# Optimization experiments

Hardware: AMD Instinct MI355X
Metric: run time of the kernel (lower is better)

The kernel has to match this reference:

```python
import jax, jax.numpy as jnp
import numpy as np

N = 50000        # nodes
E = 600000       # edges (before self-loops)
VOCAB = 100000
EMB = 128
HID = 128
G = 64           # graphs in batch
NEG_SLOPE = 0.2


def setup_inputs() -> dict:
    key = jax.random.key(0)
    ks = jax.random.split(key, 16)
    x_idx = jax.random.randint(ks[0], (N,), 0, VOCAB)
    edge_index = jax.random.randint(ks[1], (2, E), 0, N)
    edge_attr = jax.random.uniform(ks[2], (E,), dtype=jnp.float32)
    batch = jnp.sort(jax.random.randint(ks[3], (N,), 0, G))
    # embedding table; padding_idx=0 row zeroed as in nn.Embedding(padding_idx=0)
    emb_table = (jax.random.normal(ks[4], (VOCAB, EMB), dtype=jnp.float32) * 0.05).at[0].set(0.0)
    glorot = lambda k, shp: jax.random.normal(k, shp, dtype=jnp.float32) * np.float32(np.sqrt(2.0 / sum(shp)))
    W1 = glorot(ks[5], (HID, EMB))
    att_src1 = glorot(ks[6], (HID,)) * 0.0 + jax.random.normal(ks[6], (HID,), dtype=jnp.float32) * np.float32(np.sqrt(2.0 / (HID + 1)))
    att_dst1 = jax.random.normal(ks[7], (HID,), dtype=jnp.float32) * np.float32(np.sqrt(2.0 / (HID + 1)))
    W2 = glorot(ks[8], (HID, HID))
    att_src2 = jax.random.normal(ks[9], (HID,), dtype=jnp.float32) * np.float32(np.sqrt(2.0 / (HID + 1)))
    att_dst2 = jax.random.normal(ks[10], (HID,), dtype=jnp.float32) * np.float32(np.sqrt(2.0 / (HID + 1)))
    W3 = glorot(ks[11], (HID // 2, HID))
    b3 = jnp.zeros((HID // 2,), jnp.float32)
    W4 = glorot(ks[12], (2, HID // 2))
    b4 = jnp.zeros((2,), jnp.float32)
    return {"x_idx": x_idx, "edge_index": edge_index, "edge_attr": edge_attr, "batch": batch,
            "emb_table": emb_table, "W1": W1, "att_src1": att_src1, "att_dst1": att_dst1,
            "W2": W2, "att_src2": att_src2, "att_dst2": att_dst2,
            "W3": W3, "b3": b3, "W4": W4, "b4": b4}


def _segment_softmax(logits, seg, n):
    m = jax.ops.segment_max(logits, seg, num_segments=n)
    e = jnp.exp(logits - m[seg])
    s = jax.ops.segment_sum(e, seg, num_segments=n)
    return e / (s[seg] + 1e-16)


def _edge_attr_gat_conv(x, src, dst, ea, W, a_src, a_dst, n):
    H = x @ W.T                                   # [n, out]
    # per-edge score: (H_i . a_dst) + (H_j . a_src); compute per-node then gather
    alpha = (H @ a_dst)[dst] + (H @ a_src)[src]   # [e]
    alpha = jnp.where(alpha >= 0, alpha, NEG_SLOPE * alpha)
    alpha = alpha * ea                            # multiplicative edge attr
    alpha = _segment_softmax(alpha, dst, n)       # softmax over in-neighborhoods
    return jax.ops.segment_sum(H[src] * alpha[:, None], dst, num_segments=n)


def reference(x_idx, edge_index, edge_attr, batch, emb_table,
              W1, att_src1, att_dst1, W2, att_src2, att_dst2, W3, b3, W4, b4):
    n = x_idx.shape[0]
    loops = jnp.arange(n)
    # add_self_loops (done inside each conv in torch; same edges both layers)
    src = jnp.concatenate([edge_index[0], loops])
    dst = jnp.concatenate([edge_index[1], loops])  # edge_index_i (aggregation index)
    ea = jnp.concatenate([edge_attr, jnp.ones((n,), edge_attr.dtype)])
    x = emb_table[x_idx]
    x = jax.nn.relu(_edge_attr_gat_conv(x, src, dst, ea, W1, att_src1, att_dst1, n))
    x = jax.nn.relu(_edge_attr_gat_conv(x, src, dst, ea, W2, att_src2, att_dst2, n))
    # global_mean_pool
    sums = jax.ops.segment_sum(x, batch, num_segments=G)
    counts = jax.ops.segment_sum(jnp.ones((n,), x.dtype), batch, num_segments=G)
    g = sums / jnp.maximum(counts, 1.0)[:, None]
    # MLP head (dropout = identity at eval)
    h = jax.nn.relu(g @ W3.T + b3)
    return h @ W4.T + b4
```

## Files before the change

### kernel.cpp

```cpp
#include <hip/hip_runtime.h>
#include <cstdint>
#include <cstddef>


#define CSR_CHUNK 8192
#define NXCD 8

__device__ __forceinline__ float wave_sum(float v) {
#pragma unroll
  for (int m = 32; m >= 1; m >>= 1) v += __shfl_xor(v, m, 64);
  return v;
}


__global__ void init_kernel(int* __restrict__ deg, float* __restrict__ gsum,
                            int* __restrict__ gstart, int* __restrict__ gend,
                            int N, int G) {
  int i = blockIdx.x * blockDim.x + threadIdx.x;
  if (i < N) deg[i] = 1;
  if (i < G * 128) gsum[i] = 0.f;
  if (i < G) { gstart[i] = 0; gend[i] = 0; }
}

__global__ void count_deg_part_kernel(const int* __restrict__ edge_index,
                                      int* __restrict__ deg, int E, int RN) {
  int r = blockIdx.x & (NXCD - 1);
  int s = blockIdx.x >> 3;
  int lo = r * RN, hi = lo + RN;
  int e1 = min(E, (s + 1) * CSR_CHUNK);
  for (int e = s * CSR_CHUNK + threadIdx.x; e < e1; e += blockDim.x) {
    int d = edge_index[E + e];
    if (d >= lo && d < hi) atomicAdd(&deg[d], 1);
  }
}

__global__ void scan1_kernel(const int* __restrict__ deg, int* __restrict__ bsum, int N) {
  __shared__ int ws[4];
  int tid = threadIdx.x;
  int i = blockIdx.x * 256 + tid;
  int v = (i < N) ? deg[i] : 0;
#pragma unroll
  for (int m = 32; m >= 1; m >>= 1) v += __shfl_xor(v, m, 64);
  if ((tid & 63) == 0) ws[tid >> 6] = v;
  __syncthreads();
  if (tid == 0) bsum[blockIdx.x] = ws[0] + ws[1] + ws[2] + ws[3];
}

__device__ __forceinline__ int block_excl_scan_256(int v, int tid, int* wsum) {
  int lane = tid & 63, wid = tid >> 6;
  int incl = v;
#pragma unroll
  for (int off = 1; off < 64; off <<= 1) {
    int t = __shfl_up(incl, off, 64);
    if (lane >= off) incl += t;
  }
  if (lane == 63) wsum[wid] = incl;
  __syncthreads();
  int woff = 0;
#pragma unroll
  for (int w = 0; w < 4; ++w)
    if (w < wid) woff += wsum[w];
  return woff + incl - v;
}

__global__ void scan2_kernel(const int* __restrict__ bsum, int* __restrict__ boff,
                             int* __restrict__ row_ptr, int nb, int N) {
  __shared__ int wsum[4];
  int tid = threadIdx.x;
  int v = (tid < nb) ? bsum[tid] : 0;
  int excl = block_excl_scan_256(v, tid, wsum);
  if (tid < nb) boff[tid] = excl;
  if (tid == 255) row_ptr[N] = excl + v;
}

__global__ void scan3_fill_kernel(const int* __restrict__ deg, const int* __restrict__ boff,
                                  int* __restrict__ row_ptr, int2* __restrict__ pk,
                                  int* __restrict__ cur, int N) {
  __shared__ int wsum[4];
  int tid = threadIdx.x;
  int i = blockIdx.x * 256 + tid;
  int v = (i < N) ? deg[i] : 0;
  int excl = block_excl_scan_256(v, tid, wsum);
  if (i < N) {
    int p = boff[blockIdx.x] + excl;
    row_ptr[i] = p;
    pk[p] = make_int2(i, __float_as_int(1.0f));
    cur[i] = p + 1;
  }
}

__global__ void fillB_part_kernel(const int* __restrict__ edge_index,
                                  const float* __restrict__ ea,
                                  int* __restrict__ cur, int2* __restrict__ pk,
                                  int E, int RN) {
  int r = blockIdx.x & (NXCD - 1);
  int s = blockIdx.x >> 3;
  int lo = r * RN, hi = lo + RN;
  int e1 = min(E, (s + 1) * CSR_CHUNK);
  for (int e = s * CSR_CHUNK + threadIdx.x; e < e1; e += blockDim.x) {
    int d = edge_index[E + e];
    if (d >= lo && d < hi) {
      int s0 = edge_index[e];
      float a0 = ea[e];
      int p = atomicAdd(&cur[d], 1);
      pk[p] = make_int2(s0, __float_as_int(a0));
    }
  }
}


__global__ __launch_bounds__(256) void gemm_att_kernel(
    const float* __restrict__ Xin, const int* __restrict__ gidx,
    const float* __restrict__ W,
    const float* __restrict__ a_src, const float* __restrict__ a_dst,
    float* __restrict__ H, float* __restrict__ sv, float* __restrict__ dv, int N) {
  __shared__ float XsT[32][64];
  __shared__ float Wt[32][128];
  __shared__ float av[2][128];

  int tid = threadIdx.x;
  int tx = tid & 15, ty = tid >> 4;
  int rb = blockIdx.x * 64;

  if (tid < 128) { av[0][tid] = a_src[tid]; av[1][tid] = a_dst[tid]; }

  int r0 = tid & 63;
  int q0 = tid >> 6;
  int gr0 = rb + r0; if (gr0 >= N) gr0 = N - 1;
  const float* rp0 = gidx ? (Xin + (size_t)gidx[gr0] * 128) : (Xin + (size_t)gr0 * 128);

  float acc[4][8];
#pragma unroll
  for (int r = 0; r < 4; ++r)
#pragma unroll
    for (int j = 0; j < 8; ++j) acc[r][j] = 0.f;

#pragma unroll
  for (int ks = 0; ks < 4; ++ks) {
    const int k0 = ks * 32;
    __syncthreads();
    {
      float4 v0 = *(const float4*)(rp0 + k0 + q0 * 4);
      float4 v1 = *(const float4*)(rp0 + k0 + (q0 + 4) * 4);
      XsT[q0 * 4 + 0][r0] = v0.x; XsT[q0 * 4 + 1][r0] = v0.y;
      XsT[q0 * 4 + 2][r0] = v0.z; XsT[q0 * 4 + 3][r0] = v0.w;
      XsT[(q0 + 4) * 4 + 0][r0] = v1.x; XsT[(q0 + 4) * 4 + 1][r0] = v1.y;
      XsT[(q0 + 4) * 4 + 2][r0] = v1.z; XsT[(q0 + 4) * 4 + 3][r0] = v1.w;
    }
#pragma unroll
    for (int it = 0; it < 4; ++it) {
      int idx = tid + it * 256;
      int c = idx & 127, q = idx >> 7;
      float4 v = *(const float4*)(W + (size_t)c * 128 + k0 + q * 4);
      Wt[q * 4 + 0][c] = v.x; Wt[q * 4 + 1][c] = v.y;
      Wt[q * 4 + 2][c] = v.z; Wt[q * 4 + 3][c] = v.w;
    }
    __syncthreads();
#pragma unroll 8
    for (int k = 0; k < 32; ++k) {
      float4 xa = *(const float4*)&XsT[k][ty * 4];
      float4 wl = *(const float4*)&Wt[k][tx * 4];
      float4 wh = *(const float4*)&Wt[k][tx * 4 + 64];
      float xr[4] = {xa.x, xa.y, xa.z, xa.w};
      float wv[8] = {wl.x, wl.y, wl.z, wl.w, wh.x, wh.y, wh.z, wh.w};
#pragma unroll
      for (int r = 0; r < 4; ++r)
#pragma unroll
        for (int j = 0; j < 8; ++j) acc[r][j] = fmaf(xr[r], wv[j], acc[r][j]);
    }
  }

#pragma unroll
  for (int r = 0; r < 4; ++r) {
    int gr = rb + ty * 4 + r;
    float ps = 0.f, pd = 0.f;
#pragma unroll
    for (int j = 0; j < 4; ++j) {
      ps = fmaf(acc[r][j], av[0][tx * 4 + j], ps);
      ps = fmaf(acc[r][4 + j], av[0][tx * 4 + 64 + j], ps);
      pd = fmaf(acc[r][j], av[1][tx * 4 + j], pd);
      pd = fmaf(acc[r][4 + j], av[1][tx * 4 + 64 + j], pd);
    }
#pragma unroll
    for (int m = 1; m < 16; m <<= 1) {
      ps += __shfl_xor(ps, m, 64);
      pd += __shfl_xor(pd, m, 64);
    }
    if (gr < N) {
      float4 lo = make_float4(acc[r][0], acc[r][1], acc[r][2], acc[r][3]);
      float4 hi = make_float4(acc[r][4], acc[r][5], acc[r][6], acc[r][7]);
      *(float4*)(H + (size_t)gr * 128 + tx * 4) = lo;
      *(float4*)(H + (size_t)gr * 128 + 64 + tx * 4) = hi;
      if (tx == 0) { sv[gr] = ps; dv[gr] = pd; }
    }
  }
}


__global__ __launch_bounds__(256) void agg_kernel(
    const float* __restrict__ H, const float* __restrict__ sv, const float* __restrict__ dv,
    const int* __restrict__ row_ptr, const int2* __restrict__ pk,
    float* __restrict__ Xout, int N) {
  int tid = threadIdx.x;
  int hw = tid >> 5;
  int cl = tid & 31;
  int node = blockIdx.x * 8 + hw;
  if (node >= N) return;
  int p0 = row_ptr[node], p1 = row_ptr[node + 1];
  int deg = p1 - p0;
  float di = dv[node];

  float4 acc = make_float4(0.f, 0.f, 0.f, 0.f);
  float S = 0.f;

  if (deg <= 32) {
    float f = -3.4e38f; int sE = 0;
    if (cl < deg) {
      int2 pe = pk[p0 + cl];
      sE = pe.x;
      float t = di + sv[sE];
      t = (t >= 0.f) ? t : 0.2f * t;
      f = t * __int_as_float(pe.y);
    }
    float m = f;
#pragma unroll
    for (int s = 16; s >= 1; s >>= 1) m = fmaxf(m, __shfl_xor(m, s, 32));
    float w = (cl < deg) ? expf(f - m) : 0.f;
    float Ss = w;
#pragma unroll
    for (int s = 16; s >= 1; s >>= 1) Ss += __shfl_xor(Ss, s, 32);
    S = Ss;
    for (int t0 = 0; t0 < deg; t0 += 4) {
      float4 v[4]; float wv[4];
#pragma unroll
      for (int u = 0; u < 4; ++u) {
        int idx = t0 + u;
        float wj = __shfl(w, idx, 32);
        int sj = __shfl(sE, idx, 32);
        bool valid = idx < deg;
        wv[u] = valid ? wj : 0.f;
        const float4* hr = (const float4*)(H + (size_t)(valid ? sj : 0) * 128);
        v[u] = hr[cl];
      }
#pragma unroll
      for (int u = 0; u < 4; ++u) {
        acc.x = fmaf(wv[u], v[u].x, acc.x);
        acc.y = fmaf(wv[u], v[u].y, acc.y);
        acc.z = fmaf(wv[u], v[u].z, acc.z);
        acc.w = fmaf(wv[u], v[u].w, acc.w);
      }
    }
  } else {
    float m = -3.4e38f;
    for (int p = p0; p < p1; p += 32) {
      int e = p + cl;
      float f = -3.4e38f;
      if (e < p1) {
        int2 pe = pk[e];
        float t = di + sv[pe.x];
        t = (t >= 0.f) ? t : 0.2f * t;
        f = t * __int_as_float(pe.y);
      }
#pragma unroll
      for (int s = 16; s >= 1; s >>= 1) f = fmaxf(f, __shfl_xor(f, s, 32));
      m = fmaxf(m, f);
    }
    for (int p = p0; p < p1; p += 32) {
      int cnt = min(32, p1 - p);
      float w = 0.f; int sE = 0;
      if (cl < cnt) {
        int2 pe = pk[p + cl];
        sE = pe.x;
        float t = di + sv[sE];
        t = (t >= 0.f) ? t : 0.2f * t;
        w = expf(t * __int_as_float(pe.y) - m);
      }
      float Ss = w;
#pragma unroll
      for (int s = 16; s >= 1; s >>= 1) Ss += __shfl_xor(Ss, s, 32);
      S += Ss;
      for (int t0 = 0; t0 < cnt; t0 += 4) {
        float4 v[4]; float wv[4];
#pragma unroll
        for (int u = 0; u < 4; ++u) {
          int idx = t0 + u;
          float wj = __shfl(w, idx, 32);
          int sj = __shfl(sE, idx, 32);
          bool valid = idx < cnt;
          wv[u] = valid ? wj : 0.f;
          const float4* hr = (const float4*)(H + (size_t)(valid ? sj : 0) * 128);
          v[u] = hr[cl];
        }
#pragma unroll
        for (int u = 0; u < 4; ++u) {
          acc.x = fmaf(wv[u], v[u].x, acc.x);
          acc.y = fmaf(wv[u], v[u].y, acc.y);
          acc.z = fmaf(wv[u], v[u].z, acc.z);
          acc.w = fmaf(wv[u], v[u].w, acc.w);
        }
      }
    }
  }

  float sc = 1.0f / (S + 1e-16f);
  float4 o;
  o.x = fmaxf(acc.x * sc, 0.f);
  o.y = fmaxf(acc.y * sc, 0.f);
  o.z = fmaxf(acc.z * sc, 0.f);
  o.w = fmaxf(acc.w * sc, 0.f);
  *(float4*)(Xout + (size_t)node * 128 + cl * 4) = o;
}


__global__ void batch_bounds_kernel(const int* __restrict__ batch,
                                    int* __restrict__ gstart, int* __restrict__ gend, int N) {
  int i = blockIdx.x * blockDim.x + threadIdx.x;
  if (i >= N) return;
  int b = batch[i];
  if (i == 0 || batch[i - 1] != b) gstart[b] = i;
  if (i == N - 1 || batch[i + 1] != b) gend[b] = i + 1;
}

__global__ void pool_kernel(const float* __restrict__ X, const int* __restrict__ batch,
                            float* __restrict__ gsum, int N) {
  int col = threadIdx.x & 127;
  int half = threadIdx.x >> 7;
  int base = blockIdx.x * 128;
  int cur = -1; float acc = 0.f;
  for (int j = half; j < 128; j += 2) {
    int n = base + j;
    if (n >= N) break;
    int g = batch[n];
    if (g != cur) {
      if (cur >= 0) atomicAdd(&gsum[cur * 128 + col], acc);
      cur = g; acc = 0.f;
    }
    acc += X[(size_t)n * 128 + col];
  }
  if (cur >= 0) atomicAdd(&gsum[cur * 128 + col], acc);
}

__global__ __launch_bounds__(256) void head_kernel(
    const float* __restrict__ gsum,
    const int* __restrict__ gstart, const int* __restrict__ gend,
    const float* __restrict__ W3, const float* __restrict__ b3,
    const float* __restrict__ W4, const float* __restrict__ b4,
    float* __restrict__ out, int G) {
  __shared__ float gv[128];
  __shared__ float h[64];
  int gid = blockIdx.x;
  int tid = threadIdx.x;
  float cnt = (float)(gend[gid] - gstart[gid]);
  if (cnt < 1.f) cnt = 1.f;
  if (tid < 128) gv[tid] = gsum[(size_t)gid * 128 + tid] / cnt;
  __syncthreads();
  {
    int c = tid >> 2, part = tid & 3;
    const float4* w = (const float4*)(W3 + (size_t)c * 128 + part * 32);
    const float4* gg = (const float4*)(gv + part * 32);
    float acc = 0.f;
#pragma unroll
    for (int k = 0; k < 8; ++k) {
      float4 a = gg[k], b = w[k];
      acc = fmaf(a.x, b.x, acc); acc = fmaf(a.y, b.y, acc);
      acc = fmaf(a.z, b.z, acc); acc = fmaf(a.w, b.w, acc);
    }
    acc += __shfl_xor(acc, 1, 64);
    acc += __shfl_xor(acc, 2, 64);
    if (part == 0) { float v = acc + b3[c]; h[c] = (v > 0.f) ? v : 0.f; }
  }
  __syncthreads();
  if (tid < 128) {
    int o = tid >> 6, k = tid & 63;
    float p = h[k] * W4[o * 64 + k];
    p = wave_sum(p);
    if (k == 0) out[gid * 2 + o] = p + b4[o];
  }
}


extern "C" void kernel_launch(void* const* d_in, const int* in_sizes, int n_in,
                              void* d_out, int out_size, void* d_ws, size_t ws_size,
                              hipStream_t stream) {
  const int* x_idx = (const int*)d_in[0];
  const int* edge_index = (const int*)d_in[1];
  const float* edge_attr = (const float*)d_in[2];
  const int* batch = (const int*)d_in[3];
  const float* emb = (const float*)d_in[4];
  const float* W1 = (const float*)d_in[5];
  const float* as1 = (const float*)d_in[6];
  const float* ad1 = (const float*)d_in[7];
  const float* W2 = (const float*)d_in[8];
  const float* as2 = (const float*)d_in[9];
  const float* ad2 = (const float*)d_in[10];
  const float* W3 = (const float*)d_in[11];
  const float* b3 = (const float*)d_in[12];
  const float* W4 = (const float*)d_in[13];
  const float* b4 = (const float*)d_in[14];

  const int N = in_sizes[0];
  const int E = in_sizes[2];
  const int G = out_size / 2;
  const int ET = E + N;

  uint8_t* wp = (uint8_t*)d_ws;
  auto take = [&](size_t bytes) -> void* {
    void* p = (void*)wp;
    wp += (bytes + 255) & ~(size_t)255;
    return p;
  };
  float* H    = (float*)take((size_t)N * 128 * 4);
  float* X    = (float*)take((size_t)N * 128 * 4);
  float* sv   = (float*)take((size_t)N * 4);
  float* dv   = (float*)take((size_t)N * 4);
  int*   deg  = (int*)take((size_t)N * 4);
  int*   rowp = (int*)take((size_t)(N + 1) * 4);
  int*   cur  = (int*)take((size_t)N * 4);
  int*   bsum = (int*)take(256 * 4);
  int*   boff = (int*)take(256 * 4);
  int2*  pk   = (int2*)take((size_t)ET * 8);
  float* gsum = (float*)take((size_t)G * 128 * 4);
  int*   gstart = (int*)take((size_t)G * 4);
  int*   gend   = (int*)take((size_t)G * 4);
  (void)ws_size; (void)n_in;

  const int nb = (N + 255) / 256;
  const int RN = (N + NXCD - 1) / NXCD;
  const int ns = (E + CSR_CHUNK - 1) / CSR_CHUNK;
  const int pb = ns * NXCD;

  init_kernel<<<nb, 256, 0, stream>>>(deg, gsum, gstart, gend, N, G);
  count_deg_part_kernel<<<pb, 256, 0, stream>>>(edge_index, deg, E, RN);
  scan1_kernel<<<nb, 256, 0, stream>>>(deg, bsum, N);
  scan2_kernel<<<1, 256, 0, stream>>>(bsum, boff, rowp, nb, N);
  scan3_fill_kernel<<<nb, 256, 0, stream>>>(deg, boff, rowp, pk, cur, N);
  fillB_part_kernel<<<pb, 256, 0, stream>>>(edge_index, edge_attr, cur, pk, E, RN);

  const int gb = (N + 63) / 64;
  const int ab = (N + 7) / 8;
  gemm_att_kernel<<<gb, 256, 0, stream>>>(emb, x_idx, W1, as1, ad1, H, sv, dv, N);
  agg_kernel<<<ab, 256, 0, stream>>>(H, sv, dv, rowp, pk, X, N);
  gemm_att_kernel<<<gb, 256, 0, stream>>>(X, nullptr, W2, as2, ad2, H, sv, dv, N);
  agg_kernel<<<ab, 256, 0, stream>>>(H, sv, dv, rowp, pk, X, N);
  batch_bounds_kernel<<<nb, 256, 0, stream>>>(batch, gstart, gend, N);
  pool_kernel<<<(N + 127) / 128, 256, 0, stream>>>(X, batch, gsum, N);
  head_kernel<<<G, 256, 0, stream>>>(gsum, gstart, gend, W3, b3, W4, b4, (float*)d_out, G);
}
```

Measured before the change: 273.1 us.

## Enlarge GEMM tile to 128 rows with 8x8 per-thread micro-tile; fold batch bounds into init

```diff
diff --git a/kernel.cpp b/kernel.cpp
--- a/kernel.cpp
+++ b/kernel.cpp
@@ -14,12 +14,17 @@
 
 
 __global__ void init_kernel(int* __restrict__ deg, float* __restrict__ gsum,
+                            const int* __restrict__ batch,
                             int* __restrict__ gstart, int* __restrict__ gend,
                             int N, int G) {
   int i = blockIdx.x * blockDim.x + threadIdx.x;
-  if (i < N) deg[i] = 1;
+  if (i < N) {
+    deg[i] = 1;
+    int b = batch[i];
+    if (i == 0 || batch[i - 1] != b) gstart[b] = i;
+    if (i == N - 1 || batch[i + 1] != b) gend[b] = i + 1;
+  }
   if (i < G * 128) gsum[i] = 0.f;
-  if (i < G) { gstart[i] = 0; gend[i] = 0; }
 }
 
 __global__ void count_deg_part_kernel(const int* __restrict__ edge_index,
@@ -114,24 +119,25 @@
     const float* __restrict__ W,
     const float* __restrict__ a_src, const float* __restrict__ a_dst,
     float* __restrict__ H, float* __restrict__ sv, float* __restrict__ dv, int N) {
-  __shared__ float XsT[32][64];
+  __shared__ float XsT[32][128];
   __shared__ float Wt[32][128];
   __shared__ float av[2][128];
 
   int tid = threadIdx.x;
   int tx = tid & 15, ty = tid >> 4;
-  int rb = blockIdx.x * 64;
+  int rb = blockIdx.x * 128;
 
   if (tid < 128) { av[0][tid] = a_src[tid]; av[1][tid] = a_dst[tid]; }
 
-  int r0 = tid & 63;
-  int q0 = tid >> 6;
+  int r0 = tid & 127;
+  int q0 = tid >> 7;
   int gr0 = rb + r0; if (gr0 >= N) gr0 = N - 1;
   const float* rp0 = gidx ? (Xin + (size_t)gidx[gr0] * 128) : (Xin + (size_t)gr0 * 128);
-
-  float acc[4][8];
-#pragma unroll
-  for (int r = 0; r < 4; ++r)
+  const float* wp0 = W + (size_t)r0 * 128;
+
+  float acc[8][8];
+#pragma unroll
+  for (int r = 0; r < 8; ++r)
 #pragma unroll
     for (int j = 0; j < 8; ++j) acc[r][j] = 0.f;
 
@@ -139,47 +145,40 @@
   for (int ks = 0; ks < 4; ++ks) {
     const int k0 = ks * 32;
     __syncthreads();
-    {
-      float4 v0 = *(const float4*)(rp0 + k0 + q0 * 4);
-      float4 v1 = *(const float4*)(rp0 + k0 + (q0 + 4) * 4);
-      XsT[q0 * 4 + 0][r0] = v0.x; XsT[q0 * 4 + 1][r0] = v0.y;
-      XsT[q0 * 4 + 2][r0] = v0.z; XsT[q0 * 4 + 3][r0] = v0.w;
-      XsT[(q0 + 4) * 4 + 0][r0] = v1.x; XsT[(q0 + 4) * 4 + 1][r0] = v1.y;
-      XsT[(q0 + 4) * 4 + 2][r0] = v1.z; XsT[(q0 + 4) * 4 + 3][r0] = v1.w;
-    }
 #pragma unroll
     for (int it = 0; it < 4; ++it) {
-      int idx = tid + it * 256;
-      int c = idx & 127, q = idx >> 7;
-      float4 v = *(const float4*)(W + (size_t)c * 128 + k0 + q * 4);
-      Wt[q * 4 + 0][c] = v.x; Wt[q * 4 + 1][c] = v.y;
-      Wt[q * 4 + 2][c] = v.z; Wt[q * 4 + 3][c] = v.w;
+      int q = q0 + it * 2;
+      float4 v = *(const float4*)(rp0 + k0 + q * 4);
+      XsT[q * 4 + 0][r0] = v.x; XsT[q * 4 + 1][r0] = v.y;
+      XsT[q * 4 + 2][r0] = v.z; XsT[q * 4 + 3][r0] = v.w;
+      float4 u = *(const float4*)(wp0 + k0 + q * 4);
+      Wt[q * 4 + 0][r0] = u.x; Wt[q * 4 + 1][r0] = u.y;
+      Wt[q * 4 + 2][r0] = u.z; Wt[q * 4 + 3][r0] = u.w;
     }
     __syncthreads();
-#pragma unroll 8
+#pragma unroll 2
     for (int k = 0; k < 32; ++k) {
-      float4 xa = *(const float4*)&XsT[k][ty * 4];
-      float4 wl = *(const float4*)&Wt[k][tx * 4];
-      float4 wh = *(const float4*)&Wt[k][tx * 4 + 64];
-      float xr[4] = {xa.x, xa.y, xa.z, xa.w};
-      float wv[8] = {wl.x, wl.y, wl.z, wl.w, wh.x, wh.y, wh.z, wh.w};
-#pragma unroll
-      for (int r = 0; r < 4; ++r)
-#pragma unroll
-        for (int j = 0; j < 8; ++j) acc[r][j] = fmaf(xr[r], wv[j], acc[r][j]);
-    }
-  }
-
-#pragma unroll
-  for (int r = 0; r < 4; ++r) {
-    int gr = rb + ty * 4 + r;
+      float4 xa0 = *(const float4*)&XsT[k][ty * 8];
+      float4 xa1 = *(const float4*)&XsT[k][ty * 8 + 4];
+      float4 wb0 = *(const float4*)&Wt[k][tx * 8];
+      float4 wb1 = *(const float4*)&Wt[k][tx * 8 + 4];
+      float xr[8] = {xa0.x, xa0.y, xa0.z, xa0.w, xa1.x, xa1.y, xa1.z, xa1.w};
+      float wc[8] = {wb0.x, wb0.y, wb0.z, wb0.w, wb1.x, wb1.y, wb1.z, wb1.w};
+#pragma unroll
+      for (int r = 0; r < 8; ++r)
+#pragma unroll
+        for (int j = 0; j < 8; ++j) acc[r][j] = fmaf(xr[r], wc[j], acc[r][j]);
+    }
+  }
+
+#pragma unroll
+  for (int r = 0; r < 8; ++r) {
+    int gr = rb + ty * 8 + r;
     float ps = 0.f, pd = 0.f;
 #pragma unroll
-    for (int j = 0; j < 4; ++j) {
-      ps = fmaf(acc[r][j], av[0][tx * 4 + j], ps);
-      ps = fmaf(acc[r][4 + j], av[0][tx * 4 + 64 + j], ps);
-      pd = fmaf(acc[r][j], av[1][tx * 4 + j], pd);
-      pd = fmaf(acc[r][4 + j], av[1][tx * 4 + 64 + j], pd);
+    for (int j = 0; j < 8; ++j) {
+      ps = fmaf(acc[r][j], av[0][tx * 8 + j], ps);
+      pd = fmaf(acc[r][j], av[1][tx * 8 + j], pd);
     }
 #pragma unroll
     for (int m = 1; m < 16; m <<= 1) {
@@ -189,8 +188,8 @@
     if (gr < N) {
       float4 lo = make_float4(acc[r][0], acc[r][1], acc[r][2], acc[r][3]);
       float4 hi = make_float4(acc[r][4], acc[r][5], acc[r][6], acc[r][7]);
-      *(float4*)(H + (size_t)gr * 128 + tx * 4) = lo;
-      *(float4*)(H + (size_t)gr * 128 + 64 + tx * 4) = hi;
+      *(float4*)(H + (size_t)gr * 128 + tx * 8) = lo;
+      *(float4*)(H + (size_t)gr * 128 + tx * 8 + 4) = hi;
       if (tx == 0) { sv[gr] = ps; dv[gr] = pd; }
     }
   }
@@ -311,15 +310,6 @@
   *(float4*)(Xout + (size_t)node * 128 + cl * 4) = o;
 }
 
-
-__global__ void batch_bounds_kernel(const int* __restrict__ batch,
-                                    int* __restrict__ gstart, int* __restrict__ gend, int N) {
-  int i = blockIdx.x * blockDim.x + threadIdx.x;
-  if (i >= N) return;
-  int b = batch[i];
-  if (i == 0 || batch[i - 1] != b) gstart[b] = i;
-  if (i == N - 1 || batch[i + 1] != b) gend[b] = i + 1;
-}
 
 __global__ void pool_kernel(const float* __restrict__ X, const int* __restrict__ batch,
                             float* __restrict__ gsum, int N) {
@@ -429,20 +419,19 @@
   const int ns = (E + CSR_CHUNK - 1) / CSR_CHUNK;
   const int pb = ns * NXCD;
 
-  init_kernel<<<nb, 256, 0, stream>>>(deg, gsum, gstart, gend, N, G);
+  init_kernel<<<nb, 256, 0, stream>>>(deg, gsum, batch, gstart, gend, N, G);
   count_deg_part_kernel<<<pb, 256, 0, stream>>>(edge_index, deg, E, RN);
   scan1_kernel<<<nb, 256, 0, stream>>>(deg, bsum, N);
   scan2_kernel<<<1, 256, 0, stream>>>(bsum, boff, rowp, nb, N);
   scan3_fill_kernel<<<nb, 256, 0, stream>>>(deg, boff, rowp, pk, cur, N);
   fillB_part_kernel<<<pb, 256, 0, stream>>>(edge_index, edge_attr, cur, pk, E, RN);
 
-  const int gb = (N + 63) / 64;
+  const int gb = (N + 127) / 128;
   const int ab = (N + 7) / 8;
   gemm_att_kernel<<<gb, 256, 0, stream>>>(emb, x_idx, W1, as1, ad1, H, sv, dv, N);
   agg_kernel<<<ab, 256, 0, stream>>>(H, sv, dv, rowp, pk, X, N);
   gemm_att_kernel<<<gb, 256, 0, stream>>>(X, nullptr, W2, as2, ad2, H, sv, dv, N);
   agg_kernel<<<ab, 256, 0, stream>>>(H, sv, dv, rowp, pk, X, N);
-  batch_bounds_kernel<<<nb, 256, 0, stream>>>(batch, gstart, gend, N);
   pool_kernel<<<(N + 127) / 128, 256, 0, stream>>>(X, batch, gsum, N);
   head_kernel<<<G, 256, 0, stream>>>(gsum, gstart, gend, W3, b3, W4, b4, (float*)d_out, G);
 }
```

New measurement: 274.6 us. Within noise of the previous version (+0.5%).
